# Performance work log

Measured on AMD Instinct MI355X. Metric: run time of the kernel, lower is better.

Reference implementation:

```python
import jax, jax.numpy as jnp
import numpy as np

B = 65536      # groups per batch
S = 4          # members per group (target_size in source)
D = 256        # embedding_dim
NU = 200000    # num_users
NI = 100000    # num_items
NG = 50000     # num_groups


def setup_inputs() -> dict:
    key = jax.random.key(0)
    ks = jax.random.split(key, 18)
    inp = {
        'group_inputs': jax.random.randint(ks[0], (B,), 0, NG),
        'item_inputs': jax.random.randint(ks[1], (B,), 0, NI),
        'group_members': jax.random.randint(ks[2], (NG, S), 0, NU),
        'user_emb': jax.random.normal(ks[3], (NU, D), jnp.float32) * 0.05,
        'item_emb': jax.random.normal(ks[4], (NI, D), jnp.float32) * 0.05,
        'group_emb': jax.random.normal(ks[5], (NG, D), jnp.float32) * 0.05,
        'att_w1': jax.random.normal(ks[6], (2 * D, 16), jnp.float32) * 0.05,
        'att_b1': jnp.zeros((16,), jnp.float32),
        'att_w2': jax.random.normal(ks[7], (16, 1), jnp.float32) * 0.05,
        'att_b2': jnp.zeros((1,), jnp.float32),
        'cls_w': jax.random.normal(ks[8], (1, 2), jnp.float32),
        'cls_b': jnp.zeros((2,), jnp.float32),
        'pred_w1': jax.random.normal(ks[9], (3 * D, 8), jnp.float32) * 0.05,
        'pred_b1': jnp.zeros((8,), jnp.float32),
        'pred_w2': jax.random.normal(ks[10], (8, 1), jnp.float32) * 0.05,
        'pred_b2': jnp.zeros((1,), jnp.float32),
    }
    return inp


def reference(group_inputs, item_inputs, group_members,
              user_emb, item_emb, group_emb,
              att_w1, att_b1, att_w2, att_b2,
              cls_w, cls_b, pred_w1, pred_b1, pred_w2, pred_b2):
    # gather member ids per group: [B, S]
    mem_idx = group_members[group_inputs]
    members = user_emb[mem_idx]                    # [B, S, D]
    items = item_emb[item_inputs]                  # [B, D]
    items_rep = jnp.broadcast_to(items[:, None, :], members.shape)
    gi = jnp.concatenate([members, items_rep], axis=-1)  # [B, S, 2D]

    # attention MLP: 2D -> 16 -> 1, softmax over members
    h = jax.nn.relu(jnp.einsum('bse,ef->bsf', gi, att_w1) + att_b1)
    logits = (jnp.einsum('bsf,fo->bso', h, att_w2) + att_b2)[..., 0]  # [B, S]
    at_wt = jax.nn.softmax(logits, axis=1)

    max_idx = jnp.argmax(at_wt, axis=1)            # [B]

    # classifier Linear(1,2) applied per attention weight -> [B, S, 2]
    scores = at_wt[..., None] * cls_w[0] + cls_b
    classes = jnp.argmax(scores, axis=-1)          # argmax(softmax)=argmax, [B, S]
    # group-level class = class of the max-weight member
    pred_class = jnp.take_along_axis(classes, max_idx[:, None], axis=1)[:, 0]  # [B]

    # branch: gather argmax member (leader) vs attention-weighted sum
    leader = jnp.take_along_axis(members, max_idx[:, None, None], axis=1)[:, 0, :]
    weighted = jnp.einsum('bs,bsd->bd', at_wt, members)
    g_att = jnp.where((pred_class == 1)[:, None], leader, weighted)

    g = g_att + group_emb[group_inputs]            # [B, D]
    elem = g * items
    new = jnp.concatenate([elem, g, items], axis=-1)   # [B, 3D]
    y = jax.nn.sigmoid(jax.nn.relu(new @ pred_w1 + pred_b1) @ pred_w2 + pred_b2)
    return y, at_wt, pred_class.astype(jnp.float32)
```

## Files before the change

kernel.cpp:

```cpp
#include <hip/hip_runtime.h>

#define NB 65536
#define GPB 8

__device__ __forceinline__ float rs8v(float v0, float v1, float v2, float v3,
                                      float v4, float v5, float v6, float v7,
                                      bool b0, bool b1, bool b2) {
    float s, r;
    s = b0 ? v0 : v4; r = __shfl_xor(s, 1); float w0 = (b0 ? v4 : v0) + r;
    s = b0 ? v1 : v5; r = __shfl_xor(s, 1); float w1 = (b0 ? v5 : v1) + r;
    s = b0 ? v2 : v6; r = __shfl_xor(s, 1); float w2 = (b0 ? v6 : v2) + r;
    s = b0 ? v3 : v7; r = __shfl_xor(s, 1); float w3 = (b0 ? v7 : v3) + r;
    s = b1 ? w0 : w2; r = __shfl_xor(s, 2); float x0 = (b1 ? w2 : w0) + r;
    s = b1 ? w1 : w3; r = __shfl_xor(s, 2); float x1 = (b1 ? w3 : w1) + r;
    s = b2 ? x0 : x1; r = __shfl_xor(s, 4); float u = (b2 ? x1 : x0) + r;
    u += __shfl_xor(u, 8);
    u += __shfl_xor(u, 16);
    return u;
}

__global__ __launch_bounds__(256) void agree_kernel(
    const int* __restrict__ group_inputs,
    const int* __restrict__ item_inputs,
    const int* __restrict__ group_members,
    const float* __restrict__ user_emb,
    const float* __restrict__ item_emb,
    const float* __restrict__ group_emb,
    const float* __restrict__ att_w1,
    const float* __restrict__ att_b1,
    const float* __restrict__ att_w2,
    const float* __restrict__ att_b2,
    const float* __restrict__ cls_w,
    const float* __restrict__ cls_b,
    const float* __restrict__ pred_w1,
    const float* __restrict__ pred_b1,
    const float* __restrict__ pred_w2,
    const float* __restrict__ pred_b2,
    float* __restrict__ out)
{
    __shared__ __align__(16) float sBuf[32 * 260];

    const int tid = threadIdx.x;
    const int t = tid & 31;
    const int b = blockIdx.x * GPB + (tid >> 5);

    const int g  = group_inputs[b];
    const int it = item_inputs[b];
    const int4 mem = ((const int4*)group_members)[g];

    float mbr[4][8];
    {
        const int mi[4] = {mem.x, mem.y, mem.z, mem.w};
        #pragma unroll
        for (int s = 0; s < 4; ++s) {
            const float4* p = (const float4*)user_emb + (((long)mi[s]) << 6) + (t << 1);
            float4 v0 = p[0], v1 = p[1];
            mbr[s][0] = v0.x; mbr[s][1] = v0.y; mbr[s][2] = v0.z; mbr[s][3] = v0.w;
            mbr[s][4] = v1.x; mbr[s][5] = v1.y; mbr[s][6] = v1.z; mbr[s][7] = v1.w;
        }
    }
    float itv[8];
    {
        const float4* p = (const float4*)item_emb + (((long)it) << 6) + (t << 1);
        float4 v0 = p[0], v1 = p[1];
        itv[0] = v0.x; itv[1] = v0.y; itv[2] = v0.z; itv[3] = v0.w;
        itv[4] = v1.x; itv[5] = v1.y; itv[6] = v1.z; itv[7] = v1.w;
    }

    const bool b0 = (t & 1), b1 = (t & 2), b2 = (t & 4);
    const int fstar = ((t & 1) << 2) + (t & 2) + ((t >> 2) & 1);
    const float ab1_0 = att_b1[fstar],     ab1_1 = att_b1[8 + fstar];
    const float aw2_0 = att_w2[fstar],     aw2_1 = att_w2[8 + fstar];
    const float pb1v  = pred_b1[fstar],    pw2v  = pred_w2[fstar];
    const float pb2v  = pred_b2[0];
    const float cw0 = cls_w[0], cw1 = cls_w[1], cb0 = cls_b[0], cb1 = cls_b[1];

    {
        const float4* src = (const float4*)att_w1;
        for (int i = tid; i < 2048; i += 256) {
            float4 v = src[i];
            int r = i >> 2, cb = (i & 3) << 2;
            *(float4*)(sBuf + 260 * (r >> 4) + ((r & 15) << 4) + cb) = v;
        }
    }
    __syncthreads();

    const float* mbase = sBuf + 260 * (t >> 1) + ((t & 1) << 7);
    const float* ibase = mbase + 260 * 16;
    float logit[4] = {0.f, 0.f, 0.f, 0.f};
    #pragma unroll
    for (int fh = 0; fh < 2; ++fh) {
        float acc[4][8], pi[8];
        #pragma unroll
        for (int f = 0; f < 8; ++f) {
            pi[f] = 0.f;
            #pragma unroll
            for (int s = 0; s < 4; ++s) acc[s][f] = 0.f;
        }
        const float* mb = mbase + (fh << 3);
        const float* ib = ibase + (fh << 3);
        #pragma unroll
        for (int j = 0; j < 8; ++j) {
            float4 wa = *(const float4*)(mb + (j << 4));
            float4 wb = *(const float4*)(mb + (j << 4) + 4);
            float4 wc = *(const float4*)(ib + (j << 4));
            float4 wd = *(const float4*)(ib + (j << 4) + 4);
            #pragma unroll
            for (int s = 0; s < 4; ++s) {
                float mv = mbr[s][j];
                acc[s][0] += mv * wa.x; acc[s][1] += mv * wa.y;
                acc[s][2] += mv * wa.z; acc[s][3] += mv * wa.w;
                acc[s][4] += mv * wb.x; acc[s][5] += mv * wb.y;
                acc[s][6] += mv * wb.z; acc[s][7] += mv * wb.w;
            }
            float iv = itv[j];
            pi[0] += iv * wc.x; pi[1] += iv * wc.y; pi[2] += iv * wc.z; pi[3] += iv * wc.w;
            pi[4] += iv * wd.x; pi[5] += iv * wd.y; pi[6] += iv * wd.z; pi[7] += iv * wd.w;
        }
        float piR = rs8v(pi[0], pi[1], pi[2], pi[3], pi[4], pi[5], pi[6], pi[7],
                         b0, b1, b2);
        float hb  = piR + (fh ? ab1_1 : ab1_0);
        float w2v = fh ? aw2_1 : aw2_0;
        #pragma unroll
        for (int s = 0; s < 4; ++s) {
            float h = rs8v(acc[s][0], acc[s][1], acc[s][2], acc[s][3],
                           acc[s][4], acc[s][5], acc[s][6], acc[s][7],
                           b0, b1, b2) + hb;
            logit[s] += fmaxf(h, 0.f) * w2v;
        }
    }
    #pragma unroll
    for (int s = 0; s < 4; ++s) {
        float v = logit[s];
        v += __shfl_xor(v, 1); v += __shfl_xor(v, 2); v += __shfl_xor(v, 4);
        logit[s] = v;
    }

    float l0 = logit[0], l1 = logit[1], l2 = logit[2], l3 = logit[3];
    float mx = fmaxf(fmaxf(l0, l1), fmaxf(l2, l3));
    float e0 = __expf(l0 - mx), e1 = __expf(l1 - mx);
    float e2 = __expf(l2 - mx), e3 = __expf(l3 - mx);
    float den = e0 + e1 + e2 + e3;
    float at0 = e0 / den, at1 = e1 / den, at2 = e2 / den, at3 = e3 / den;

    int best = 0; float bv = at0;
    if (at1 > bv) { bv = at1; best = 1; }
    if (at2 > bv) { bv = at2; best = 2; }
    if (at3 > bv) { bv = at3; best = 3; }
    int pc = (bv * cw1 + cb1) > (bv * cw0 + cb0) ? 1 : 0;

    float gvr[8];
    {
        const float4* p = (const float4*)group_emb + (((long)g) << 6) + (t << 1);
        float4 v0 = p[0], v1 = p[1];
        gvr[0] = v0.x; gvr[1] = v0.y; gvr[2] = v0.z; gvr[3] = v0.w;
        gvr[4] = v1.x; gvr[5] = v1.y; gvr[6] = v1.z; gvr[7] = v1.w;
    }

    __syncthreads();
    {
        const float4* srcp = (const float4*)pred_w1;
        for (int i = tid; i < 1536; i += 256) {
            float4 v = srcp[i];
            int r = i >> 1, cb = (i & 1) << 2;
            *(float4*)(sBuf + 132 * (r >> 4) + ((r & 15) << 3) + cb) = v;
        }
    }

    float gvec[8], elv[8];
    #pragma unroll
    for (int d = 0; d < 8; ++d) {
        float w = at0 * mbr[0][d] + at1 * mbr[1][d] + at2 * mbr[2][d] + at3 * mbr[3][d];
        float ldr = mbr[0][d];
        ldr = (best == 1) ? mbr[1][d] : ldr;
        ldr = (best == 2) ? mbr[2][d] : ldr;
        ldr = (best == 3) ? mbr[3][d] : ldr;
        float ga = pc ? ldr : w;
        float gg = ga + gvr[d];
        gvec[d] = gg;
        elv[d]  = gg * itv[d];
    }
    __syncthreads();

    const float* pbase = sBuf + 132 * (t >> 1) + ((t & 1) << 6);
    float po[8] = {0.f,0.f,0.f,0.f,0.f,0.f,0.f,0.f};
    #pragma unroll
    for (int j = 0; j < 8; ++j) {
        const float* pA = pbase + (j << 3);
        float4 a0 = *(const float4*)pA,          a1 = *(const float4*)(pA + 4);
        float4 g0 = *(const float4*)(pA + 2112), g1 = *(const float4*)(pA + 2116);
        float4 c0 = *(const float4*)(pA + 4224), c1 = *(const float4*)(pA + 4228);
        float e = elv[j], gg = gvec[j], iv = itv[j];
        po[0] += e * a0.x; po[0] += gg * g0.x; po[0] += iv * c0.x;
        po[1] += e * a0.y; po[1] += gg * g0.y; po[1] += iv * c0.y;
        po[2] += e * a0.z; po[2] += gg * g0.z; po[2] += iv * c0.z;
        po[3] += e * a0.w; po[3] += gg * g0.w; po[3] += iv * c0.w;
        po[4] += e * a1.x; po[4] += gg * g1.x; po[4] += iv * c1.x;
        po[5] += e * a1.y; po[5] += gg * g1.y; po[5] += iv * c1.y;
        po[6] += e * a1.z; po[6] += gg * g1.z; po[6] += iv * c1.z;
        po[7] += e * a1.w; po[7] += gg * g1.w; po[7] += iv * c1.w;
    }
    float poR = rs8v(po[0], po[1], po[2], po[3], po[4], po[5], po[6], po[7],
                     b0, b1, b2);
    float z = fmaxf(poR + pb1v, 0.f) * pw2v;
    z += __shfl_xor(z, 1); z += __shfl_xor(z, 2); z += __shfl_xor(z, 4);
    z += pb2v;
    float y = 1.f / (1.f + __expf(-z));

    if (t == 0) {
        out[b] = y;
        *(float4*)(out + NB + 4 * b) = make_float4(at0, at1, at2, at3);
        out[5 * NB + b] = (float)pc;
    }
}

extern "C" void kernel_launch(void* const* d_in, const int* in_sizes, int n_in,
                              void* d_out, int out_size, void* d_ws, size_t ws_size,
                              hipStream_t stream) {
    (void)in_sizes; (void)n_in; (void)out_size; (void)d_ws; (void)ws_size;
    agree_kernel<<<NB / GPB, 256, 0, stream>>>(
        (const int*)d_in[0], (const int*)d_in[1], (const int*)d_in[2],
        (const float*)d_in[3], (const float*)d_in[4], (const float*)d_in[5],
        (const float*)d_in[6], (const float*)d_in[7], (const float*)d_in[8],
        (const float*)d_in[9], (const float*)d_in[10], (const float*)d_in[11],
        (const float*)d_in[12], (const float*)d_in[13], (const float*)d_in[14],
        (const float*)d_in[15], (float*)d_out);
}
```

Baseline: 445.3 us.

## Process two groups per 32-lane slice to reuse shared-memory weight loads

Each 32-thread slice now handles two batch rows instead of one, and blocks cover 16 groups. Each weight float4 read from shared memory is reused across both groups, and more gathers are in flight per thread. The attention MLP is re-tiled into four 4-feature passes with a new 4-way shuffle reduction, which keeps the accumulator count bounded. The cost is higher register pressure, from two rows of member embeddings and accumulators, which may lower occupancy. There are also half as many blocks, which amortises the per-block weight staging.

```diff
diff --git a/kernel.cpp b/kernel.cpp
--- a/kernel.cpp
+++ b/kernel.cpp
@@ -1,7 +1,19 @@
 #include <hip/hip_runtime.h>
 
 #define NB 65536
-#define GPB 8
+#define GPB 16
+
+__device__ __forceinline__ float rs4v(float v0, float v1, float v2, float v3,
+                                      bool b0, bool b1) {
+    float s, r;
+    s = b0 ? v0 : v2; r = __shfl_xor(s, 1); float w0 = (b0 ? v2 : v0) + r;
+    s = b0 ? v1 : v3; r = __shfl_xor(s, 1); float w1 = (b0 ? v3 : v1) + r;
+    s = b1 ? w0 : w1; r = __shfl_xor(s, 2); float u  = (b1 ? w1 : w0) + r;
+    u += __shfl_xor(u, 4);
+    u += __shfl_xor(u, 8);
+    u += __shfl_xor(u, 16);
+    return u;
+}
 
 __device__ __forceinline__ float rs8v(float v0, float v1, float v2, float v3,
                                       float v4, float v5, float v6, float v7,
@@ -42,38 +54,50 @@
 
     const int tid = threadIdx.x;
     const int t = tid & 31;
-    const int b = blockIdx.x * GPB + (tid >> 5);
-
-    const int g  = group_inputs[b];
-    const int it = item_inputs[b];
-    const int4 mem = ((const int4*)group_members)[g];
-
-    float mbr[4][8];
-    {
-        const int mi[4] = {mem.x, mem.y, mem.z, mem.w};
-        #pragma unroll
-        for (int s = 0; s < 4; ++s) {
-            const float4* p = (const float4*)user_emb + (((long)mi[s]) << 6) + (t << 1);
+    const int b0 = blockIdx.x * GPB + ((tid >> 5) << 1);
+
+    const int gA  = group_inputs[b0];
+    const int gB  = group_inputs[b0 + 1];
+    const int itA = item_inputs[b0];
+    const int itB = item_inputs[b0 + 1];
+    const int4 mA = ((const int4*)group_members)[gA];
+    const int4 mB = ((const int4*)group_members)[gB];
+
+    float mbr[2][4][8];
+    {
+        const int mi[2][4] = {{mA.x, mA.y, mA.z, mA.w}, {mB.x, mB.y, mB.z, mB.w}};
+        #pragma unroll
+        for (int gg = 0; gg < 2; ++gg) {
+            #pragma unroll
+            for (int s = 0; s < 4; ++s) {
+                const float4* p = (const float4*)user_emb + (((long)mi[gg][s]) << 6) + (t << 1);
+                float4 v0 = p[0], v1 = p[1];
+                mbr[gg][s][0] = v0.x; mbr[gg][s][1] = v0.y; mbr[gg][s][2] = v0.z; mbr[gg][s][3] = v0.w;
+                mbr[gg][s][4] = v1.x; mbr[gg][s][5] = v1.y; mbr[gg][s][6] = v1.z; mbr[gg][s][7] = v1.w;
+            }
+        }
+    }
+    float itv[2][8];
+    {
+        const int ii[2] = {itA, itB};
+        #pragma unroll
+        for (int gg = 0; gg < 2; ++gg) {
+            const float4* p = (const float4*)item_emb + (((long)ii[gg]) << 6) + (t << 1);
             float4 v0 = p[0], v1 = p[1];
-            mbr[s][0] = v0.x; mbr[s][1] = v0.y; mbr[s][2] = v0.z; mbr[s][3] = v0.w;
-            mbr[s][4] = v1.x; mbr[s][5] = v1.y; mbr[s][6] = v1.z; mbr[s][7] = v1.w;
-        }
-    }
-    float itv[8];
-    {
-        const float4* p = (const float4*)item_emb + (((long)it) << 6) + (t << 1);
-        float4 v0 = p[0], v1 = p[1];
-        itv[0] = v0.x; itv[1] = v0.y; itv[2] = v0.z; itv[3] = v0.w;
-        itv[4] = v1.x; itv[5] = v1.y; itv[6] = v1.z; itv[7] = v1.w;
-    }
-
-    const bool b0 = (t & 1), b1 = (t & 2), b2 = (t & 4);
-    const int fstar = ((t & 1) << 2) + (t & 2) + ((t >> 2) & 1);
-    const float ab1_0 = att_b1[fstar],     ab1_1 = att_b1[8 + fstar];
-    const float aw2_0 = att_w2[fstar],     aw2_1 = att_w2[8 + fstar];
-    const float pb1v  = pred_b1[fstar],    pw2v  = pred_w2[fstar];
-    const float pb2v  = pred_b2[0];
-    const float cw0 = cls_w[0], cw1 = cls_w[1], cb0 = cls_b[0], cb1 = cls_b[1];
+            itv[gg][0] = v0.x; itv[gg][1] = v0.y; itv[gg][2] = v0.z; itv[gg][3] = v0.w;
+            itv[gg][4] = v1.x; itv[gg][5] = v1.y; itv[gg][6] = v1.z; itv[gg][7] = v1.w;
+        }
+    }
+
+    const bool bb0 = (t & 1), bb1 = (t & 2), bb2 = (t & 4);
+    const int f4 = ((t & 1) << 1) | ((t >> 1) & 1);
+    const int f8 = ((t & 1) << 2) + (t & 2) + ((t >> 2) & 1);
+    float ab1v[4], aw2v[4];
+    #pragma unroll
+    for (int p = 0; p < 4; ++p) {
+        ab1v[p] = att_b1[4 * p + f4];
+        aw2v[p] = att_w2[4 * p + f4];
+    }
 
     {
         const float4* src = (const float4*)att_w1;
@@ -87,74 +111,96 @@
 
     const float* mbase = sBuf + 260 * (t >> 1) + ((t & 1) << 7);
     const float* ibase = mbase + 260 * 16;
-    float logit[4] = {0.f, 0.f, 0.f, 0.f};
-    #pragma unroll
-    for (int fh = 0; fh < 2; ++fh) {
-        float acc[4][8], pi[8];
-        #pragma unroll
-        for (int f = 0; f < 8; ++f) {
-            pi[f] = 0.f;
-            #pragma unroll
-            for (int s = 0; s < 4; ++s) acc[s][f] = 0.f;
-        }
-        const float* mb = mbase + (fh << 3);
-        const float* ib = ibase + (fh << 3);
+    float logit[2][4] = {{0.f, 0.f, 0.f, 0.f}, {0.f, 0.f, 0.f, 0.f}};
+    #pragma unroll
+    for (int p = 0; p < 4; ++p) {
+        float acc[2][4][4], pi[2][4];
+        #pragma unroll
+        for (int gg = 0; gg < 2; ++gg) {
+            #pragma unroll
+            for (int f = 0; f < 4; ++f) {
+                pi[gg][f] = 0.f;
+                #pragma unroll
+                for (int s = 0; s < 4; ++s) acc[gg][s][f] = 0.f;
+            }
+        }
         #pragma unroll
         for (int j = 0; j < 8; ++j) {
-            float4 wa = *(const float4*)(mb + (j << 4));
-            float4 wb = *(const float4*)(mb + (j << 4) + 4);
-            float4 wc = *(const float4*)(ib + (j << 4));
-            float4 wd = *(const float4*)(ib + (j << 4) + 4);
+            float4 wm = *(const float4*)(mbase + (j << 4) + (p << 2));
+            float4 wi = *(const float4*)(ibase + (j << 4) + (p << 2));
+            #pragma unroll
+            for (int gg = 0; gg < 2; ++gg) {
+                #pragma unroll
+                for (int s = 0; s < 4; ++s) {
+                    float mv = mbr[gg][s][j];
+                    acc[gg][s][0] += mv * wm.x; acc[gg][s][1] += mv * wm.y;
+                    acc[gg][s][2] += mv * wm.z; acc[gg][s][3] += mv * wm.w;
+                }
+                float iv = itv[gg][j];
+                pi[gg][0] += iv * wi.x; pi[gg][1] += iv * wi.y;
+                pi[gg][2] += iv * wi.z; pi[gg][3] += iv * wi.w;
+            }
+        }
+        #pragma unroll
+        for (int gg = 0; gg < 2; ++gg) {
+            float hb = rs4v(pi[gg][0], pi[gg][1], pi[gg][2], pi[gg][3], bb0, bb1)
+                       + ab1v[p];
             #pragma unroll
             for (int s = 0; s < 4; ++s) {
-                float mv = mbr[s][j];
-                acc[s][0] += mv * wa.x; acc[s][1] += mv * wa.y;
-                acc[s][2] += mv * wa.z; acc[s][3] += mv * wa.w;
-                acc[s][4] += mv * wb.x; acc[s][5] += mv * wb.y;
-                acc[s][6] += mv * wb.z; acc[s][7] += mv * wb.w;
-            }
-            float iv = itv[j];
-            pi[0] += iv * wc.x; pi[1] += iv * wc.y; pi[2] += iv * wc.z; pi[3] += iv * wc.w;
-            pi[4] += iv * wd.x; pi[5] += iv * wd.y; pi[6] += iv * wd.z; pi[7] += iv * wd.w;
-        }
-        float piR = rs8v(pi[0], pi[1], pi[2], pi[3], pi[4], pi[5], pi[6], pi[7],
-                         b0, b1, b2);
-        float hb  = piR + (fh ? ab1_1 : ab1_0);
-        float w2v = fh ? aw2_1 : aw2_0;
+                float h = rs4v(acc[gg][s][0], acc[gg][s][1], acc[gg][s][2], acc[gg][s][3],
+                               bb0, bb1) + hb;
+                logit[gg][s] += fmaxf(h, 0.f) * aw2v[p];
+            }
+        }
+    }
+    #pragma unroll
+    for (int gg = 0; gg < 2; ++gg) {
         #pragma unroll
         for (int s = 0; s < 4; ++s) {
-            float h = rs8v(acc[s][0], acc[s][1], acc[s][2], acc[s][3],
-                           acc[s][4], acc[s][5], acc[s][6], acc[s][7],
-                           b0, b1, b2) + hb;
-            logit[s] += fmaxf(h, 0.f) * w2v;
-        }
-    }
-    #pragma unroll
-    for (int s = 0; s < 4; ++s) {
-        float v = logit[s];
-        v += __shfl_xor(v, 1); v += __shfl_xor(v, 2); v += __shfl_xor(v, 4);
-        logit[s] = v;
-    }
-
-    float l0 = logit[0], l1 = logit[1], l2 = logit[2], l3 = logit[3];
-    float mx = fmaxf(fmaxf(l0, l1), fmaxf(l2, l3));
-    float e0 = __expf(l0 - mx), e1 = __expf(l1 - mx);
-    float e2 = __expf(l2 - mx), e3 = __expf(l3 - mx);
-    float den = e0 + e1 + e2 + e3;
-    float at0 = e0 / den, at1 = e1 / den, at2 = e2 / den, at3 = e3 / den;
-
-    int best = 0; float bv = at0;
-    if (at1 > bv) { bv = at1; best = 1; }
-    if (at2 > bv) { bv = at2; best = 2; }
-    if (at3 > bv) { bv = at3; best = 3; }
-    int pc = (bv * cw1 + cb1) > (bv * cw0 + cb0) ? 1 : 0;
-
-    float gvr[8];
-    {
-        const float4* p = (const float4*)group_emb + (((long)g) << 6) + (t << 1);
-        float4 v0 = p[0], v1 = p[1];
-        gvr[0] = v0.x; gvr[1] = v0.y; gvr[2] = v0.z; gvr[3] = v0.w;
-        gvr[4] = v1.x; gvr[5] = v1.y; gvr[6] = v1.z; gvr[7] = v1.w;
+            float v = logit[gg][s];
+            v += __shfl_xor(v, 1); v += __shfl_xor(v, 2);
+            logit[gg][s] = v;
+        }
+    }
+
+    const float cw0 = cls_w[0], cw1 = cls_w[1], cb0c = cls_b[0], cb1c = cls_b[1];
+    float at[2][4]; int bestv[2], pcv[2];
+    #pragma unroll
+    for (int gg = 0; gg < 2; ++gg) {
+        float l0 = logit[gg][0], l1 = logit[gg][1], l2 = logit[gg][2], l3 = logit[gg][3];
+        float mx = fmaxf(fmaxf(l0, l1), fmaxf(l2, l3));
+        float e0 = __expf(l0 - mx), e1 = __expf(l1 - mx);
+        float e2 = __expf(l2 - mx), e3 = __expf(l3 - mx);
+        float inv = 1.f / (e0 + e1 + e2 + e3);
+        at[gg][0] = e0 * inv; at[gg][1] = e1 * inv;
+        at[gg][2] = e2 * inv; at[gg][3] = e3 * inv;
+        int best = 0; float bv = at[gg][0];
+        if (at[gg][1] > bv) { bv = at[gg][1]; best = 1; }
+        if (at[gg][2] > bv) { bv = at[gg][2]; best = 2; }
+        if (at[gg][3] > bv) { bv = at[gg][3]; best = 3; }
+        bestv[gg] = best;
+        pcv[gg] = (bv * cw1 + cb1c) > (bv * cw0 + cb0c) ? 1 : 0;
+    }
+
+    if (t == 0) {
+        #pragma unroll
+        for (int gg = 0; gg < 2; ++gg) {
+            const int b = b0 + gg;
+            *(float4*)(out + NB + 4 * b) = make_float4(at[gg][0], at[gg][1], at[gg][2], at[gg][3]);
+            out[5 * NB + b] = (float)pcv[gg];
+        }
+    }
+
+    float gvr[2][8];
+    {
+        const int gi2[2] = {gA, gB};
+        #pragma unroll
+        for (int gg = 0; gg < 2; ++gg) {
+            const float4* p = (const float4*)group_emb + (((long)gi2[gg]) << 6) + (t << 1);
+            float4 v0 = p[0], v1 = p[1];
+            gvr[gg][0] = v0.x; gvr[gg][1] = v0.y; gvr[gg][2] = v0.z; gvr[gg][3] = v0.w;
+            gvr[gg][4] = v1.x; gvr[gg][5] = v1.y; gvr[gg][6] = v1.z; gvr[gg][7] = v1.w;
+        }
     }
 
     __syncthreads();
@@ -167,50 +213,64 @@
         }
     }
 
-    float gvec[8], elv[8];
-    #pragma unroll
-    for (int d = 0; d < 8; ++d) {
-        float w = at0 * mbr[0][d] + at1 * mbr[1][d] + at2 * mbr[2][d] + at3 * mbr[3][d];
-        float ldr = mbr[0][d];
-        ldr = (best == 1) ? mbr[1][d] : ldr;
-        ldr = (best == 2) ? mbr[2][d] : ldr;
-        ldr = (best == 3) ? mbr[3][d] : ldr;
-        float ga = pc ? ldr : w;
-        float gg = ga + gvr[d];
-        gvec[d] = gg;
-        elv[d]  = gg * itv[d];
+    float gvec[2][8], elv[2][8];
+    #pragma unroll
+    for (int gg = 0; gg < 2; ++gg) {
+        #pragma unroll
+        for (int d = 0; d < 8; ++d) {
+            float w = at[gg][0] * mbr[gg][0][d] + at[gg][1] * mbr[gg][1][d]
+                    + at[gg][2] * mbr[gg][2][d] + at[gg][3] * mbr[gg][3][d];
+            float ldr = mbr[gg][0][d];
+            ldr = (bestv[gg] == 1) ? mbr[gg][1][d] : ldr;
+            ldr = (bestv[gg] == 2) ? mbr[gg][2][d] : ldr;
+            ldr = (bestv[gg] == 3) ? mbr[gg][3][d] : ldr;
+            float ga = pcv[gg] ? ldr : w;
+            float gv = ga + gvr[gg][d];
+            gvec[gg][d] = gv;
+            elv[gg][d]  = gv * itv[gg][d];
+        }
     }
     __syncthreads();
 
+    const float pb1v = pred_b1[f8], pw2v = pred_w2[f8], pb2v = pred_b2[0];
     const float* pbase = sBuf + 132 * (t >> 1) + ((t & 1) << 6);
-    float po[8] = {0.f,0.f,0.f,0.f,0.f,0.f,0.f,0.f};
+    float po[2][8] = {{0.f,0.f,0.f,0.f,0.f,0.f,0.f,0.f},
+                      {0.f,0.f,0.f,0.f,0.f,0.f,0.f,0.f}};
     #pragma unroll
     for (int j = 0; j < 8; ++j) {
         const float* pA = pbase + (j << 3);
         float4 a0 = *(const float4*)pA,          a1 = *(const float4*)(pA + 4);
-        float4 g0 = *(const float4*)(pA + 2112), g1 = *(const float4*)(pA + 2116);
+        float4 q0 = *(const float4*)(pA + 2112), q1 = *(const float4*)(pA + 2116);
         float4 c0 = *(const float4*)(pA + 4224), c1 = *(const float4*)(pA + 4228);
-        float e = elv[j], gg = gvec[j], iv = itv[j];
-        po[0] += e * a0.x; po[0] += gg * g0.x; po[0] += iv * c0.x;
-        po[1] += e * a0.y; po[1] += gg * g0.y; po[1] += iv * c0.y;
-        po[2] += e * a0.z; po[2] += gg * g0.z; po[2] += iv * c0.z;
-        po[3] += e * a0.w; po[3] += gg * g0.w; po[3] += iv * c0.w;
-        po[4] += e * a1.x; po[4] += gg * g1.x; po[4] += iv * c1.x;
-        po[5] += e * a1.y; po[5] += gg * g1.y; po[5] += iv * c1.y;
-        po[6] += e * a1.z; po[6] += gg * g1.z; po[6] += iv * c1.z;
-        po[7] += e * a1.w; po[7] += gg * g1.w; po[7] += iv * c1.w;
-    }
-    float poR = rs8v(po[0], po[1], po[2], po[3], po[4], po[5], po[6], po[7],
-                     b0, b1, b2);
-    float z = fmaxf(poR + pb1v, 0.f) * pw2v;
-    z += __shfl_xor(z, 1); z += __shfl_xor(z, 2); z += __shfl_xor(z, 4);
-    z += pb2v;
-    float y = 1.f / (1.f + __expf(-z));
+        #pragma unroll
+        for (int gg = 0; gg < 2; ++gg) {
+            float e = elv[gg][j], gv = gvec[gg][j], iv = itv[gg][j];
+            po[gg][0] += e * a0.x; po[gg][0] += gv * q0.x; po[gg][0] += iv * c0.x;
+            po[gg][1] += e * a0.y; po[gg][1] += gv * q0.y; po[gg][1] += iv * c0.y;
+            po[gg][2] += e * a0.z; po[gg][2] += gv * q0.z; po[gg][2] += iv * c0.z;
+            po[gg][3] += e * a0.w; po[gg][3] += gv * q0.w; po[gg][3] += iv * c0.w;
+            po[gg][4] += e * a1.x; po[gg][4] += gv * q1.x; po[gg][4] += iv * c1.x;
+            po[gg][5] += e * a1.y; po[gg][5] += gv * q1.y; po[gg][5] += iv * c1.y;
+            po[gg][6] += e * a1.z; po[gg][6] += gv * q1.z; po[gg][6] += iv * c1.z;
+            po[gg][7] += e * a1.w; po[gg][7] += gv * q1.w; po[gg][7] += iv * c1.w;
+        }
+    }
+
+    float yv[2];
+    #pragma unroll
+    for (int gg = 0; gg < 2; ++gg) {
+        float poR = rs8v(po[gg][0], po[gg][1], po[gg][2], po[gg][3],
+                         po[gg][4], po[gg][5], po[gg][6], po[gg][7],
+                         bb0, bb1, bb2);
+        float z = fmaxf(poR + pb1v, 0.f) * pw2v;
+        z += __shfl_xor(z, 1); z += __shfl_xor(z, 2); z += __shfl_xor(z, 4);
+        z += pb2v;
+        yv[gg] = 1.f / (1.f + __expf(-z));
+    }
 
     if (t == 0) {
-        out[b] = y;
-        *(float4*)(out + NB + 4 * b) = make_float4(at0, at1, at2, at3);
-        out[5 * NB + b] = (float)pc;
+        out[b0]     = yv[0];
+        out[b0 + 1] = yv[1];
     }
 }
 
```

After: 448.4 us. Within noise of the previous version (+0.7%).

## Use DPP lane ops for cross-lane reductions and pad shared weight layout

Applied to the files above, without the earlier changes.

Replaces most ds_bpermute-based __shfl_xor steps in the transpose-reduce helpers with DPP quad-permute and row-rotate moves, keeping a single shuffle across the 16-lane boundary. The attention MLP is split into four passes of four hidden features, so each reduction needs fewer stages, and the lane-to-feature mapping changes to match. The shared-memory weight layouts get extra padding to cut bank conflicts. In exchange there are more passes over the weight reads and some risk in the correctness of the new lane mapping.

```diff
diff --git a/kernel.cpp b/kernel.cpp
--- a/kernel.cpp
+++ b/kernel.cpp
@@ -3,19 +3,40 @@
 #define NB 65536
 #define GPB 8
 
-__device__ __forceinline__ float rs8v(float v0, float v1, float v2, float v3,
+#define QP_X1 0xB1
+#define QP_X2 0x4E
+#define ROR4  0x124
+#define ROR8  0x128
+template<int CTRL>
+__device__ __forceinline__ float fdpp(float x) {
+    return __int_as_float(__builtin_amdgcn_mov_dpp(__float_as_int(x), CTRL, 0xF, 0xF, true));
+}
+
+__device__ __forceinline__ float rs4d(float v0, float v1, float v2, float v3,
+                                      bool b0, bool b1) {
+    float s, r;
+    s = b0 ? v0 : v2; r = fdpp<QP_X1>(s); float w0 = (b0 ? v2 : v0) + r;
+    s = b0 ? v1 : v3; r = fdpp<QP_X1>(s); float w1 = (b0 ? v3 : v1) + r;
+    s = b1 ? w0 : w1; r = fdpp<QP_X2>(s); float u  = (b1 ? w1 : w0) + r;
+    u += fdpp<ROR4>(u);
+    u += fdpp<ROR8>(u);
+    u += __shfl_xor(u, 16);
+    return u;
+}
+
+__device__ __forceinline__ float rs8d(float v0, float v1, float v2, float v3,
                                       float v4, float v5, float v6, float v7,
-                                      bool b0, bool b1, bool b2) {
+                                      bool b0, bool b1, bool b4) {
     float s, r;
-    s = b0 ? v0 : v4; r = __shfl_xor(s, 1); float w0 = (b0 ? v4 : v0) + r;
-    s = b0 ? v1 : v5; r = __shfl_xor(s, 1); float w1 = (b0 ? v5 : v1) + r;
-    s = b0 ? v2 : v6; r = __shfl_xor(s, 1); float w2 = (b0 ? v6 : v2) + r;
-    s = b0 ? v3 : v7; r = __shfl_xor(s, 1); float w3 = (b0 ? v7 : v3) + r;
-    s = b1 ? w0 : w2; r = __shfl_xor(s, 2); float x0 = (b1 ? w2 : w0) + r;
-    s = b1 ? w1 : w3; r = __shfl_xor(s, 2); float x1 = (b1 ? w3 : w1) + r;
-    s = b2 ? x0 : x1; r = __shfl_xor(s, 4); float u = (b2 ? x1 : x0) + r;
-    u += __shfl_xor(u, 8);
-    u += __shfl_xor(u, 16);
+    s = b0 ? v0 : v4; r = fdpp<QP_X1>(s); float w0 = (b0 ? v4 : v0) + r;
+    s = b0 ? v1 : v5; r = fdpp<QP_X1>(s); float w1 = (b0 ? v5 : v1) + r;
+    s = b0 ? v2 : v6; r = fdpp<QP_X1>(s); float w2 = (b0 ? v6 : v2) + r;
+    s = b0 ? v3 : v7; r = fdpp<QP_X1>(s); float w3 = (b0 ? v7 : v3) + r;
+    s = b1 ? w0 : w2; r = fdpp<QP_X2>(s); float x0 = (b1 ? w2 : w0) + r;
+    s = b1 ? w1 : w3; r = fdpp<QP_X2>(s); float x1 = (b1 ? w3 : w1) + r;
+    s = b4 ? x0 : x1; r = __shfl_xor(s, 16); float u = (b4 ? x1 : x0) + r;
+    u += fdpp<ROR4>(u);
+    u += fdpp<ROR8>(u);
     return u;
 }
 
@@ -38,7 +59,7 @@
     const float* __restrict__ pred_b2,
     float* __restrict__ out)
 {
-    __shared__ __align__(16) float sBuf[32 * 260];
+    __shared__ __align__(16) float sBuf[32 * 276];
 
     const int tid = threadIdx.x;
     const int t = tid & 31;
@@ -67,12 +88,16 @@
         itv[4] = v1.x; itv[5] = v1.y; itv[6] = v1.z; itv[7] = v1.w;
     }
 
-    const bool b0 = (t & 1), b1 = (t & 2), b2 = (t & 4);
-    const int fstar = ((t & 1) << 2) + (t & 2) + ((t >> 2) & 1);
-    const float ab1_0 = att_b1[fstar],     ab1_1 = att_b1[8 + fstar];
-    const float aw2_0 = att_w2[fstar],     aw2_1 = att_w2[8 + fstar];
-    const float pb1v  = pred_b1[fstar],    pw2v  = pred_w2[fstar];
-    const float pb2v  = pred_b2[0];
+    const bool bb0 = (t & 1), bb1 = (t & 2), bb4 = (t & 16);
+    const int f4  = ((t & 1) << 1) | ((t >> 1) & 1);
+    const int f8n = ((t & 1) << 2) + (t & 2) + ((t >> 4) & 1);
+    float ab1v[4], aw2v[4];
+    #pragma unroll
+    for (int p = 0; p < 4; ++p) {
+        ab1v[p] = att_b1[4 * p + f4];
+        aw2v[p] = att_w2[4 * p + f4];
+    }
+    const float pb1v = pred_b1[f8n], pw2v = pred_w2[f8n], pb2v = pred_b2[0];
     const float cw0 = cls_w[0], cw1 = cls_w[1], cb0 = cls_b[0], cb1 = cls_b[1];
 
     {
@@ -80,59 +105,49 @@
         for (int i = tid; i < 2048; i += 256) {
             float4 v = src[i];
             int r = i >> 2, cb = (i & 3) << 2;
-            *(float4*)(sBuf + 260 * (r >> 4) + ((r & 15) << 4) + cb) = v;
+            *(float4*)(sBuf + 276 * (r >> 4) + 144 * ((r >> 3) & 1) + ((r & 7) << 4) + cb) = v;
         }
     }
     __syncthreads();
 
-    const float* mbase = sBuf + 260 * (t >> 1) + ((t & 1) << 7);
-    const float* ibase = mbase + 260 * 16;
+    const float* mbase = sBuf + 276 * (t >> 1) + 144 * (t & 1);
+    const float* ibase = mbase + 276 * 16;
     float logit[4] = {0.f, 0.f, 0.f, 0.f};
     #pragma unroll
-    for (int fh = 0; fh < 2; ++fh) {
-        float acc[4][8], pi[8];
-        #pragma unroll
-        for (int f = 0; f < 8; ++f) {
+    for (int p = 0; p < 4; ++p) {
+        float acc[4][4], pi[4];
+        #pragma unroll
+        for (int f = 0; f < 4; ++f) {
             pi[f] = 0.f;
             #pragma unroll
             for (int s = 0; s < 4; ++s) acc[s][f] = 0.f;
         }
-        const float* mb = mbase + (fh << 3);
-        const float* ib = ibase + (fh << 3);
         #pragma unroll
         for (int j = 0; j < 8; ++j) {
-            float4 wa = *(const float4*)(mb + (j << 4));
-            float4 wb = *(const float4*)(mb + (j << 4) + 4);
-            float4 wc = *(const float4*)(ib + (j << 4));
-            float4 wd = *(const float4*)(ib + (j << 4) + 4);
+            float4 wm = *(const float4*)(mbase + (j << 4) + (p << 2));
+            float4 wi = *(const float4*)(ibase + (j << 4) + (p << 2));
             #pragma unroll
             for (int s = 0; s < 4; ++s) {
                 float mv = mbr[s][j];
-                acc[s][0] += mv * wa.x; acc[s][1] += mv * wa.y;
-                acc[s][2] += mv * wa.z; acc[s][3] += mv * wa.w;
-                acc[s][4] += mv * wb.x; acc[s][5] += mv * wb.y;
-                acc[s][6] += mv * wb.z; acc[s][7] += mv * wb.w;
+                acc[s][0] += mv * wm.x; acc[s][1] += mv * wm.y;
+                acc[s][2] += mv * wm.z; acc[s][3] += mv * wm.w;
             }
             float iv = itv[j];
-            pi[0] += iv * wc.x; pi[1] += iv * wc.y; pi[2] += iv * wc.z; pi[3] += iv * wc.w;
-            pi[4] += iv * wd.x; pi[5] += iv * wd.y; pi[6] += iv * wd.z; pi[7] += iv * wd.w;
-        }
-        float piR = rs8v(pi[0], pi[1], pi[2], pi[3], pi[4], pi[5], pi[6], pi[7],
-                         b0, b1, b2);
-        float hb  = piR + (fh ? ab1_1 : ab1_0);
-        float w2v = fh ? aw2_1 : aw2_0;
+            pi[0] += iv * wi.x; pi[1] += iv * wi.y;
+            pi[2] += iv * wi.z; pi[3] += iv * wi.w;
+        }
+        float hb = rs4d(pi[0], pi[1], pi[2], pi[3], bb0, bb1) + ab1v[p];
         #pragma unroll
         for (int s = 0; s < 4; ++s) {
-            float h = rs8v(acc[s][0], acc[s][1], acc[s][2], acc[s][3],
-                           acc[s][4], acc[s][5], acc[s][6], acc[s][7],
-                           b0, b1, b2) + hb;
-            logit[s] += fmaxf(h, 0.f) * w2v;
+            float h = rs4d(acc[s][0], acc[s][1], acc[s][2], acc[s][3], bb0, bb1) + hb;
+            logit[s] += fmaxf(h, 0.f) * aw2v[p];
         }
     }
     #pragma unroll
     for (int s = 0; s < 4; ++s) {
         float v = logit[s];
-        v += __shfl_xor(v, 1); v += __shfl_xor(v, 2); v += __shfl_xor(v, 4);
+        v += fdpp<QP_X1>(v);
+        v += fdpp<QP_X2>(v);
         logit[s] = v;
     }
 
@@ -163,7 +178,7 @@
         for (int i = tid; i < 1536; i += 256) {
             float4 v = srcp[i];
             int r = i >> 1, cb = (i & 1) << 2;
-            *(float4*)(sBuf + 132 * (r >> 4) + ((r & 15) << 3) + cb) = v;
+            *(float4*)(sBuf + 148 * (r >> 4) + 80 * ((r >> 3) & 1) + ((r & 7) << 3) + cb) = v;
         }
     }
 
@@ -182,28 +197,30 @@
     }
     __syncthreads();
 
-    const float* pbase = sBuf + 132 * (t >> 1) + ((t & 1) << 6);
+    const float* pbase = sBuf + 148 * (t >> 1) + 80 * (t & 1);
     float po[8] = {0.f,0.f,0.f,0.f,0.f,0.f,0.f,0.f};
     #pragma unroll
     for (int j = 0; j < 8; ++j) {
         const float* pA = pbase + (j << 3);
         float4 a0 = *(const float4*)pA,          a1 = *(const float4*)(pA + 4);
-        float4 g0 = *(const float4*)(pA + 2112), g1 = *(const float4*)(pA + 2116);
-        float4 c0 = *(const float4*)(pA + 4224), c1 = *(const float4*)(pA + 4228);
+        float4 q0 = *(const float4*)(pA + 2368), q1 = *(const float4*)(pA + 2372);
+        float4 c0 = *(const float4*)(pA + 4736), c1 = *(const float4*)(pA + 4740);
         float e = elv[j], gg = gvec[j], iv = itv[j];
-        po[0] += e * a0.x; po[0] += gg * g0.x; po[0] += iv * c0.x;
-        po[1] += e * a0.y; po[1] += gg * g0.y; po[1] += iv * c0.y;
-        po[2] += e * a0.z; po[2] += gg * g0.z; po[2] += iv * c0.z;
-        po[3] += e * a0.w; po[3] += gg * g0.w; po[3] += iv * c0.w;
-        po[4] += e * a1.x; po[4] += gg * g1.x; po[4] += iv * c1.x;
-        po[5] += e * a1.y; po[5] += gg * g1.y; po[5] += iv * c1.y;
-        po[6] += e * a1.z; po[6] += gg * g1.z; po[6] += iv * c1.z;
-        po[7] += e * a1.w; po[7] += gg * g1.w; po[7] += iv * c1.w;
-    }
-    float poR = rs8v(po[0], po[1], po[2], po[3], po[4], po[5], po[6], po[7],
-                     b0, b1, b2);
+        po[0] += e * a0.x; po[0] += gg * q0.x; po[0] += iv * c0.x;
+        po[1] += e * a0.y; po[1] += gg * q0.y; po[1] += iv * c0.y;
+        po[2] += e * a0.z; po[2] += gg * q0.z; po[2] += iv * c0.z;
+        po[3] += e * a0.w; po[3] += gg * q0.w; po[3] += iv * c0.w;
+        po[4] += e * a1.x; po[4] += gg * q1.x; po[4] += iv * c1.x;
+        po[5] += e * a1.y; po[5] += gg * q1.y; po[5] += iv * c1.y;
+        po[6] += e * a1.z; po[6] += gg * q1.z; po[6] += iv * c1.z;
+        po[7] += e * a1.w; po[7] += gg * q1.w; po[7] += iv * c1.w;
+    }
+    float poR = rs8d(po[0], po[1], po[2], po[3], po[4], po[5], po[6], po[7],
+                     bb0, bb1, bb4);
     float z = fmaxf(poR + pb1v, 0.f) * pw2v;
-    z += __shfl_xor(z, 1); z += __shfl_xor(z, 2); z += __shfl_xor(z, 4);
+    z += fdpp<QP_X1>(z);
+    z += fdpp<QP_X2>(z);
+    z += __shfl_xor(z, 16);
     z += pb2v;
     float y = 1.f / (1.f + __expf(-z));
 
```

Result: faster. 427.4 us (-4.0%).
